# Kernel tuning notes

Hardware: AMD Instinct MI355X
Metric: run time of the kernel (lower is better)

## Reference

```python
import jax, jax.numpy as jnp
import numpy as np

INPUT_DIM = 784
HIDDEN = 4096
BATCH = 64
T = 30                      # time_steps
TAU = 100.0                 # tau_mem
DECAY = 1.0 - 1.0 / TAU     # LIF leak per step
THR = 0.5                   # spike threshold
SCALE = 16.0                # input_scale
K = int(HIDDEN * 0.08)      # k-WTA k = hidden_dim * sparsity = 327


def setup_inputs() -> dict:
    key = jax.random.key(0)
    k1, k2, k3 = jax.random.split(key, 3)
    x = jax.random.uniform(k1, (BATCH, INPUT_DIM), dtype=jnp.float32)
    W1 = jax.random.normal(k2, (INPUT_DIM, HIDDEN), dtype=jnp.float32) * 0.05
    W2 = jax.random.normal(k3, (HIDDEN, HIDDEN), dtype=jnp.float32) * 0.02
    return {"x": x, "W1": W1, "W2": W2}


def _kwta(s):
    # k-WTA: keep units >= k-th largest value per row (binary spikes -> this
    # matches torch.topk kth-value thresholding; if row sum==0 it's a no-op).
    vals = jax.lax.top_k(s, K)[0]           # [B, K]
    thresh = vals[:, -1:]                   # [B, 1]
    return s * (s >= thresh).astype(s.dtype)


def _lif(v, cur):
    # Leaky integrate-and-fire: decay, integrate, hard-threshold, reset-to-zero.
    v = v * DECAY + cur
    s = (v >= THR).astype(v.dtype)
    return v * (1.0 - s), s


def reference(x, W1, W2):
    # prepare_input: normalize by max and scale (x.max()>0 branch)
    x = x / jnp.maximum(jnp.max(x), jnp.float32(1e-12)) * SCALE
    B = x.shape[0]

    def step(carry, _):
        v0, v1, v2, sum0, sum1, sum2 = carry
        v0, s0 = _lif(v0, x)                # Retina: external current each step
        v1, s1 = _lif(v1, s0 @ W1)          # V1 feedforward
        v2, s2 = _lif(v2, s1 @ W2)          # V2 feedforward
        s1m = _kwta(s1)                     # k-WTA applied to returned spikes
        s2m = _kwta(s2)
        return (v0, v1, v2, sum0 + s0, sum1 + s1m, sum2 + s2m), None

    z0 = jnp.zeros((B, INPUT_DIM), jnp.float32)
    zh = jnp.zeros((B, HIDDEN), jnp.float32)
    carry = (z0, zh, zh, z0, zh, zh)
    (_, _, _, sum0, sum1, sum2), _ = jax.lax.scan(step, carry, None, length=T)
    # mean firing rates per group (spike_sums / time_steps)
    return (sum0 / T, sum1 / T, sum2 / T)
```

## Files before the change

kernel.cpp:

```cpp
#include <hip/hip_runtime.h>
#include <cstdint>
#include <cstddef>

#define INPUT_DIM 784
#define HIDDEN    4096
#define BATCH     64
#define T_STEPS   30
#define N0 (BATCH*INPUT_DIM)
#define N1 (BATCH*HIDDEN)
#define M_ROWS (T_STEPS*BATCH)
#define NDIG 4
#define MB_CNT (M_ROWS/32)
#define KC1 25
#define KC2 128

typedef int v4i  __attribute__((ext_vector_type(4)));
typedef int v16i __attribute__((ext_vector_type(16)));

__global__ __launch_bounds__(256) void max_kernel(const float* __restrict__ x,
                                                  unsigned* __restrict__ maxbits) {
    int i = blockIdx.x * 256 + threadIdx.x;
    float v = (i < N0) ? x[i] : 0.0f;
    #pragma unroll
    for (int off = 32; off > 0; off >>= 1)
        v = fmaxf(v, __shfl_down(v, off, 64));
    __shared__ float sm[4];
    int lane = threadIdx.x & 63;
    int wv   = threadIdx.x >> 6;
    if (lane == 0) sm[wv] = v;
    __syncthreads();
    if (threadIdx.x == 0) {
        float m = fmaxf(fmaxf(sm[0], sm[1]), fmaxf(sm[2], sm[3]));
        atomicMax(maxbits, __float_as_uint(m));
    }
}

__global__ __launch_bounds__(256) void lif0_kernel(const float* __restrict__ x,
                                                   const unsigned* __restrict__ maxbits,
                                                   uint8_t* __restrict__ AF1,
                                                   float* __restrict__ out0) {
    int j = blockIdx.x * 256 + threadIdx.x;
    int b = blockIdx.y;
    if (j >= INPUT_DIM) return;
    float mx = fmaxf(__uint_as_float(*maxbits), 1e-12f);
    float xs = __fmul_rn(__fdiv_rn(x[b * INPUT_DIM + j], mx), 16.0f);
    int kc = j >> 5;
    int lane = (b & 31) | (((j >> 4) & 1) << 5);
    size_t base = (((size_t)(kc * MB_CNT + (b >> 5)) * 64 + lane) << 4) + (j & 15);
    float v = 0.0f;
    int cnt = 0;
    #pragma unroll
    for (int t = 0; t < T_STEPS; ++t) {
        v = __fadd_rn(__fmul_rn(v, 0.99f), xs);
        int s = (v >= 0.5f) ? 1 : 0;
        cnt += s;
        v = s ? 0.0f : v;
        AF1[base + (size_t)t * 2048] = (uint8_t)s;
    }
    out0[b * INPUT_DIM + j] = (float)cnt / 30.0f;
}

__global__ __launch_bounds__(256) void digitize_kernel(const float* __restrict__ W,
                                                       int8_t* __restrict__ BF,
                                                       int Krows, int KC, double scale) {
    __shared__ float tile[32][33];
    const int nb = blockIdx.x, kc = blockIdx.y;
    const int tid = threadIdx.x;
    {
        int r  = tid >> 3;
        int c4 = (tid & 7) << 2;
        int k  = kc * 32 + r;
        float4 w4 = make_float4(0.f, 0.f, 0.f, 0.f);
        if (k < Krows)
            w4 = *(const float4*)&W[(size_t)k * HIDDEN + nb * 32 + c4];
        tile[r][c4]     = w4.x;
        tile[r][c4 + 1] = w4.y;
        tile[r][c4 + 2] = w4.z;
        tile[r][c4 + 3] = w4.w;
    }
    __syncthreads();
    const int d    = tid >> 6;
    const int lane = tid & 63;
    const int nl   = lane & 31;
    const int kh   = (lane >> 5) << 4;
    char dig[16];
    #pragma unroll
    for (int jj = 0; jj < 16; ++jj) {
        double w = (double)tile[kh + jj][nl];
        long long q = __double2ll_rn(w * scale);
        int dd = 0;
        #pragma unroll
        for (int dd_i = 0; dd_i <= 3; ++dd_i) {
            dd = (int)(((q + 128) & 255) - 128);
            q = (q - (long long)dd) >> 8;
            if (dd_i == d) break;
        }
        dig[jj] = (char)dd;
    }
    *(int4*)&BF[((((size_t)nb * KC + kc) * NDIG + d) << 10) + (lane << 4)] =
        *(int4*)&dig[0];
}

#define MFMA_GRP(A0, A1, B0, B1, B2, B3)                                        \
    acc[0][0] = __builtin_amdgcn_mfma_i32_32x32x32_i8(A0, B0, acc[0][0], 0, 0, 0); \
    acc[1][0] = __builtin_amdgcn_mfma_i32_32x32x32_i8(A1, B0, acc[1][0], 0, 0, 0); \
    acc[0][1] = __builtin_amdgcn_mfma_i32_32x32x32_i8(A0, B1, acc[0][1], 0, 0, 0); \
    acc[1][1] = __builtin_amdgcn_mfma_i32_32x32x32_i8(A1, B1, acc[1][1], 0, 0, 0); \
    acc[0][2] = __builtin_amdgcn_mfma_i32_32x32x32_i8(A0, B2, acc[0][2], 0, 0, 0); \
    acc[1][2] = __builtin_amdgcn_mfma_i32_32x32x32_i8(A1, B2, acc[1][2], 0, 0, 0); \
    acc[0][3] = __builtin_amdgcn_mfma_i32_32x32x32_i8(A0, B3, acc[0][3], 0, 0, 0); \
    acc[1][3] = __builtin_amdgcn_mfma_i32_32x32x32_i8(A1, B3, acc[1][3], 0, 0, 0)

__device__ __forceinline__ void gload16(const int8_t* g, int8_t* l) {
    __builtin_amdgcn_global_load_lds(
        (const __attribute__((address_space(1))) void*)g,
        (__attribute__((address_space(3))) void*)l, 16, 0, 0);
}

#define STAGE(BUF, KCV)                                                          \
    do {                                                                         \
        gload16(gA  + (size_t)(KCV) * astride, &lds[BUF][       (wave << 10)]);  \
        gload16(gB0 + (size_t)(KCV) * bstride, &lds[BUF][4096 + (wave << 10)]);  \
        gload16(gB1 + (size_t)(KCV) * bstride, &lds[BUF][8192 + (wave << 10)]);  \
    } while (0)

#define ITER(S, WN, DOSTAGE, KCV)                                                \
    do {                                                                         \
        asm volatile("s_waitcnt vmcnt(" #WN ")" ::: "memory");                   \
        __builtin_amdgcn_s_barrier();                                            \
        v4i a0 = *(const v4i*)&lds[S][ msb      * 1024 + (lane << 4)];           \
        v4i a1 = *(const v4i*)&lds[S][(msb + 1) * 1024 + (lane << 4)];           \
        v4i b0 = *(const v4i*)&lds[S][4096 + ((wave & 1) << 12) +        (lane << 4)]; \
        v4i b1 = *(const v4i*)&lds[S][4096 + ((wave & 1) << 12) + 1024 + (lane << 4)]; \
        v4i b2 = *(const v4i*)&lds[S][4096 + ((wave & 1) << 12) + 2048 + (lane << 4)]; \
        v4i b3 = *(const v4i*)&lds[S][4096 + ((wave & 1) << 12) + 3072 + (lane << 4)]; \
        asm volatile("s_waitcnt lgkmcnt(0)" ::: "memory");                       \
        __builtin_amdgcn_s_barrier();                                            \
        if (DOSTAGE) { STAGE(S, (KCV) + 2); }                                    \
        MFMA_GRP(a0, a1, b0, b1, b2, b3);                                        \
    } while (0)

template <int KC>
__global__ __launch_bounds__(256, 2) void gemm_i8_kernel(const int8_t* __restrict__ AF,
                                                         const int8_t* __restrict__ BF,
                                                         double* __restrict__ C,
                                                         double scale) {
    __shared__ int8_t lds[2][12288];
    const int tid  = threadIdx.x;
    const int wave = tid >> 6, lane = tid & 63;
    const int i  = blockIdx.x;
    const int p  = (i >= 480) ? 1 : 0;
    const int j  = i - p * 480;
    const int bx = j >> 5;
    const int by = p * 32 + ((j & 7) << 2) + ((j >> 3) & 3);
    const int nb0 = by * 2;
    const int msb = (wave >> 1) * 2;

    const int astride = MB_CNT * 1024;
    const int bstride = NDIG * 1024;
    const int8_t* gA  = AF + (((size_t)(bx * 4) * 64) << 4) + tid * 16;
    const int8_t* gB0 = BF + (((size_t)nb0 * KC * NDIG) << 10) + tid * 16;
    const int8_t* gB1 = gB0 + ((size_t)KC * NDIG << 10);

    v16i acc[2][4] = {};

    STAGE(0, 0);
    STAGE(1, 1);

    constexpr int KCM = (KC - 2) & ~1;
    for (int kc = 0; kc < KCM; kc += 2) {
        ITER(0, 3, 1, kc);
        ITER(1, 3, 1, kc + 1);
    }
    if constexpr ((KC & 1) == 0) {
        ITER(0, 3, 0, KC - 2);
        ITER(1, 0, 0, KC - 1);
    } else {
        ITER(0, 3, 1, KC - 3);
        ITER(1, 3, 0, KC - 2);
        ITER(0, 0, 0, KC - 1);
    }

    const int col = lane & 31;
    const int rb  = (lane >> 5) << 2;
    const int n_g = by * 64 + (wave & 1) * 32 + col;
    #pragma unroll
    for (int s = 0; s < 2; ++s) {
        const int m_base = bx * 128 + (msb + s) * 32;
        #pragma unroll
        for (int r = 0; r < 16; ++r) {
            int row = (r & 3) + 8 * (r >> 2) + rb;
            long long v = 0;
            #pragma unroll
            for (int d = 3; d >= 0; --d) v = (v << 8) + (long long)acc[s][d][r];
            C[(size_t)(m_base + row) * HIDDEN + n_g] = (double)v * scale;
        }
    }
}

__global__ __launch_bounds__(256) void lif1_kernel(const double* __restrict__ CUR,
                                                   uint8_t* __restrict__ AF,
                                                   float* __restrict__ out1) {
    int e = blockIdx.x * 256 + threadIdx.x;
    int b = e >> 12;
    int j = e & 4095;
    int kc = j >> 5;
    int lane = (b & 31) | (((j >> 4) & 1) << 5);
    size_t base = (((size_t)(kc * MB_CNT + (b >> 5)) * 64 + lane) << 4) + (j & 15);
    double v = 0.0;
    int cnt = 0;
    #pragma unroll
    for (int t = 0; t < T_STEPS; ++t) {
        double cur = CUR[(size_t)t * N1 + e];
        v = __dadd_rn(__dmul_rn(v, 0.99), cur);
        int s = (v >= 0.5) ? 1 : 0;
        cnt += s;
        v = s ? 0.0 : v;
        AF[base + (size_t)t * 2048] = (uint8_t)s;
    }
    out1[e] = (float)cnt / 30.0f;
}

__global__ __launch_bounds__(256) void lif2_kernel(const double* __restrict__ CUR,
                                                   float* __restrict__ out2) {
    int e = blockIdx.x * 256 + threadIdx.x;
    double v = 0.0;
    int cnt = 0;
    #pragma unroll
    for (int t = 0; t < T_STEPS; ++t) {
        double cur = CUR[(size_t)t * N1 + e];
        v = __dadd_rn(__dmul_rn(v, 0.99), cur);
        int s = (v >= 0.5) ? 1 : 0;
        cnt += s;
        v = s ? 0.0 : v;
    }
    out2[e] = (float)cnt / 30.0f;
}

extern "C" void kernel_launch(void* const* d_in, const int* in_sizes, int n_in,
                              void* d_out, int out_size, void* d_ws, size_t ws_size,
                              hipStream_t stream) {
    const float* x  = (const float*)d_in[0];
    const float* W1 = (const float*)d_in[1];
    const float* W2 = (const float*)d_in[2];
    float* out = (float*)d_out;
    char*  ws  = (char*)d_ws;

    const size_t AF1_SZ = (size_t)KC1 * MB_CNT * 1024;
    const size_t BF1_SZ = (size_t)128 * KC1 * NDIG * 1024;
    const size_t AF2_SZ = (size_t)KC2 * MB_CNT * 1024;
    const size_t BF2_SZ = (size_t)128 * KC2 * NDIG * 1024;
    unsigned* maxbits = (unsigned*)ws;
    uint8_t*  AF1 = (uint8_t*)(ws + 256);
    int8_t*   BF1 = (int8_t*)(AF1 + AF1_SZ);
    uint8_t*  AF2 = (uint8_t*)(BF1 + BF1_SZ);
    int8_t*   BF2 = (int8_t*)(AF2 + AF2_SZ);
    double*   CURd = (double*)((char*)BF2 + BF2_SZ);

    float* out0 = out;
    float* out1 = out + N0;
    float* out2 = out + N0 + N1;

    hipMemsetAsync(maxbits, 0, 4, stream);
    hipMemsetAsync(AF1, 0, AF1_SZ, stream);
    max_kernel <<<(N0 + 255) / 256, 256, 0, stream>>>(x, maxbits);
    lif0_kernel<<<dim3(4, BATCH), 256, 0, stream>>>(x, maxbits, AF1, out0);
    digitize_kernel<<<dim3(128, KC1), 256, 0, stream>>>(W1, BF1, INPUT_DIM, KC1,
                                                        4294967296.0);
    digitize_kernel<<<dim3(128, KC2), 256, 0, stream>>>(W2, BF2, HIDDEN, KC2,
                                                        8589934592.0);
    gemm_i8_kernel<KC1><<<960, 256, 0, stream>>>((const int8_t*)AF1, BF1, CURd,
                                                 2.3283064365386963e-10);
    lif1_kernel<<<N1 / 256, 256, 0, stream>>>(CURd, AF2, out1);
    gemm_i8_kernel<KC2><<<960, 256, 0, stream>>>((const int8_t*)AF2, BF2, CURd,
                                                 1.1641532182693481e-10);
    lif2_kernel<<<N1 / 256, 256, 0, stream>>>(CURd, out2);
}
```

Before: 305.6 us.

## Triple-buffer int8 GEMM LDS pipeline with two k-chunks per barrier

Restructures the int8 MFMA GEMM main loop from a double-buffered one-chunk-per-iteration scheme into a triple-buffered scheme that stages two k-chunks per buffer. Each barrier now covers twice the MFMA work, and the extra buffer lets global-to-LDS loads run further ahead. It also drops the second barrier per iteration and raises wave priority around the MFMA groups. LDS use grows from 24 KB to 72 KB per block, which may limit the requested two blocks per CU. The tail handling for odd chunk counts is more complex.

```diff
diff --git a/kernel.cpp b/kernel.cpp
--- a/kernel.cpp
+++ b/kernel.cpp
@@ -117,27 +117,45 @@
         (__attribute__((address_space(3))) void*)l, 16, 0, 0);
 }
 
-#define STAGE(BUF, KCV)                                                          \
+#define STAGE1(SUBP)                                                             \
     do {                                                                         \
-        gload16(gA  + (size_t)(KCV) * astride, &lds[BUF][       (wave << 10)]);  \
-        gload16(gB0 + (size_t)(KCV) * bstride, &lds[BUF][4096 + (wave << 10)]);  \
-        gload16(gB1 + (size_t)(KCV) * bstride, &lds[BUF][8192 + (wave << 10)]);  \
+        int8_t* sb_ = (SUBP);                                                    \
+        gload16(spA,  sb_ +        (wave << 10));                                \
+        gload16(spB0, sb_ + 4096 + (wave << 10));                                \
+        gload16(spB1, sb_ + 8192 + (wave << 10));                                \
+        spA += astride; spB0 += bstride; spB1 += bstride;                        \
     } while (0)
 
-#define ITER(S, WN, DOSTAGE, KCV)                                                \
+#define STAGE2(BUF)                                                              \
     do {                                                                         \
-        asm volatile("s_waitcnt vmcnt(" #WN ")" ::: "memory");                   \
-        __builtin_amdgcn_s_barrier();                                            \
-        v4i a0 = *(const v4i*)&lds[S][ msb      * 1024 + (lane << 4)];           \
-        v4i a1 = *(const v4i*)&lds[S][(msb + 1) * 1024 + (lane << 4)];           \
-        v4i b0 = *(const v4i*)&lds[S][4096 + ((wave & 1) << 12) +        (lane << 4)]; \
-        v4i b1 = *(const v4i*)&lds[S][4096 + ((wave & 1) << 12) + 1024 + (lane << 4)]; \
-        v4i b2 = *(const v4i*)&lds[S][4096 + ((wave & 1) << 12) + 2048 + (lane << 4)]; \
-        v4i b3 = *(const v4i*)&lds[S][4096 + ((wave & 1) << 12) + 3072 + (lane << 4)]; \
-        asm volatile("s_waitcnt lgkmcnt(0)" ::: "memory");                       \
-        __builtin_amdgcn_s_barrier();                                            \
-        if (DOSTAGE) { STAGE(S, (KCV) + 2); }                                    \
-        MFMA_GRP(a0, a1, b0, b1, b2, b3);                                        \
+        STAGE1(&lds[BUF][0]);                                                    \
+        STAGE1(&lds[BUF][12288]);                                                \
+    } while (0)
+
+#define READ_FRAGS(BUF, SOFF, A0, A1, B0, B1, B2, B3)                            \
+    A0 = *(const v4i*)&lds[BUF][(SOFF) +  msb      * 1024 + (lane << 4)];        \
+    A1 = *(const v4i*)&lds[BUF][(SOFF) + (msb + 1) * 1024 + (lane << 4)];        \
+    B0 = *(const v4i*)&lds[BUF][(SOFF) + 4096 + ((wave & 1) << 12) +        (lane << 4)]; \
+    B1 = *(const v4i*)&lds[BUF][(SOFF) + 4096 + ((wave & 1) << 12) + 1024 + (lane << 4)]; \
+    B2 = *(const v4i*)&lds[BUF][(SOFF) + 4096 + ((wave & 1) << 12) + 2048 + (lane << 4)]; \
+    B3 = *(const v4i*)&lds[BUF][(SOFF) + 4096 + ((wave & 1) << 12) + 3072 + (lane << 4)]
+
+#define WAITBAR(WN)                                                              \
+    __builtin_amdgcn_sched_barrier(0);                                           \
+    asm volatile("s_waitcnt vmcnt(" #WN ")\n\ts_barrier" ::: "memory");          \
+    __builtin_amdgcn_sched_barrier(0)
+
+#define ITER2(BUF, WN, SCODE)                                                    \
+    do {                                                                         \
+        WAITBAR(WN);                                                             \
+        v4i xa0, xa1, xb0, xb1, xb2, xb3, ya0, ya1, yb0, yb1, yb2, yb3;          \
+        READ_FRAGS(BUF, 0,     xa0, xa1, xb0, xb1, xb2, xb3);                    \
+        READ_FRAGS(BUF, 12288, ya0, ya1, yb0, yb1, yb2, yb3);                    \
+        SCODE;                                                                   \
+        __builtin_amdgcn_s_setprio(1);                                           \
+        MFMA_GRP(xa0, xa1, xb0, xb1, xb2, xb3);                                  \
+        MFMA_GRP(ya0, ya1, yb0, yb1, yb2, yb3);                                  \
+        __builtin_amdgcn_s_setprio(0);                                           \
     } while (0)
 
 template <int KC>
@@ -145,7 +163,7 @@
                                                          const int8_t* __restrict__ BF,
                                                          double* __restrict__ C,
                                                          double scale) {
-    __shared__ int8_t lds[2][12288];
+    __shared__ int8_t lds[3][24576];
     const int tid  = threadIdx.x;
     const int wave = tid >> 6, lane = tid & 63;
     const int i  = blockIdx.x;
@@ -158,27 +176,43 @@
 
     const int astride = MB_CNT * 1024;
     const int bstride = NDIG * 1024;
-    const int8_t* gA  = AF + (((size_t)(bx * 4) * 64) << 4) + tid * 16;
-    const int8_t* gB0 = BF + (((size_t)nb0 * KC * NDIG) << 10) + tid * 16;
-    const int8_t* gB1 = gB0 + ((size_t)KC * NDIG << 10);
+    const int8_t* spA  = AF + (((size_t)(bx * 4) * 64) << 4) + tid * 16;
+    const int8_t* spB0 = BF + (((size_t)nb0 * KC * NDIG) << 10) + tid * 16;
+    const int8_t* spB1 = spB0 + ((size_t)KC * NDIG << 10);
 
     v16i acc[2][4] = {};
 
-    STAGE(0, 0);
-    STAGE(1, 1);
-
-    constexpr int KCM = (KC - 2) & ~1;
-    for (int kc = 0; kc < KCM; kc += 2) {
-        ITER(0, 3, 1, kc);
-        ITER(1, 3, 1, kc + 1);
-    }
-    if constexpr ((KC & 1) == 0) {
-        ITER(0, 3, 0, KC - 2);
-        ITER(1, 0, 0, KC - 1);
+    STAGE2(0);
+    STAGE2(1);
+
+    constexpr int P  = KC / 2;
+    constexpr int PM = P - 2;
+    constexpr int G  = PM / 3, R = PM % 3;
+    for (int g = 0; g < G; ++g) {
+        ITER2(0, 6, STAGE2(2));
+        ITER2(1, 6, STAGE2(0));
+        ITER2(2, 6, STAGE2(1));
+    }
+    if constexpr (R == 2) {
+        ITER2(0, 6, STAGE2(2));
+        ITER2(1, 6, STAGE2(0));
+        ITER2(2, 6, );
+        ITER2(0, 0, );
+    } else if constexpr (R == 1) {
+        ITER2(0, 6, STAGE2(2));
+        ITER2(1, 6, STAGE1(&lds[0][0]));
+        ITER2(2, 3, );
+        {
+            WAITBAR(0);
+            v4i za0, za1, zb0, zb1, zb2, zb3;
+            READ_FRAGS(0, 0, za0, za1, zb0, zb1, zb2, zb3);
+            __builtin_amdgcn_s_setprio(1);
+            MFMA_GRP(za0, za1, zb0, zb1, zb2, zb3);
+            __builtin_amdgcn_s_setprio(0);
+        }
     } else {
-        ITER(0, 3, 1, KC - 3);
-        ITER(1, 3, 0, KC - 2);
-        ITER(0, 0, 0, KC - 1);
+        ITER2(0, 6, );
+        ITER2(1, 0, );
     }
 
     const int col = lane & 31;
```

Result: slower. 325.5 us (+6.5%).
